# Performance work log

Measured on AMD Instinct MI355X. Metric: run time of the kernel, lower is better.

The kernel has to match this reference:

```python
import jax, jax.numpy as jnp
import numpy as np

B, S, E, H = 32, 512, 256, 256


def _slstm_scan(x, m, Wx, Wh, Ws, b, Us, Uh, bs):
    """x: [S,B,E], m: [S,B]. Returns per-step (h, c, s) each [S,B,H]."""
    Bn = x.shape[1]
    Hn = Wh.shape[0]
    z0 = jnp.zeros((Bn, Hn), x.dtype)

    def step(carry, xm):
        h, c, s = carry
        xt, mt = xm
        mt = mt[:, None]
        z = xt @ Wx + h @ Wh + s @ Ws + b  # [B, 4H]
        i, f, g, o = jnp.split(z, 4, axis=-1)
        c_new = jax.nn.sigmoid(f) * c + jax.nn.sigmoid(i) * jnp.tanh(g)
        h_new = jax.nn.sigmoid(o) * jnp.tanh(c_new)
        s_new = jnp.tanh(s @ Us + h_new @ Uh + bs)  # sentence-state message update
        h = mt * h_new + (1.0 - mt) * h
        c = mt * c_new + (1.0 - mt) * c
        s = mt * s_new + (1.0 - mt) * s
        return (h, c, s), (h, c, s)

    _, ys = jax.lax.scan(step, (z0, z0, z0), (x, m))
    return ys


def setup_inputs() -> dict:
    key = jax.random.key(0)
    ks = jax.random.split(key, 16)
    sc = 0.02
    d = {
        "inputs": jax.random.normal(ks[0], (B, S, E), jnp.float32),
        "mask": jnp.ones((B, S), jnp.float32),
        "idx": 1,
    }
    names = ["Wx", "Wh", "Ws", "b", "Us", "Uh", "bs"]
    shapes = [(E, 4 * H), (H, 4 * H), (H, 4 * H), (4 * H,), (H, H), (H, H), (H,)]
    k = 1
    for suf in ["_f", "_r"]:
        for n, sh in zip(names, shapes):
            d[n + suf] = sc * jax.random.normal(ks[k], sh, jnp.float32)
            k += 1
    return d


def reference(inputs, mask, idx,
              Wx_f, Wh_f, Ws_f, b_f, Us_f, Uh_f, bs_f,
              Wx_r, Wh_r, Ws_r, b_r, Us_r, Uh_r, bs_r):
    x = jnp.transpose(inputs, (1, 0, 2))  # [S,B,E]
    m = jnp.transpose(mask, (1, 0))       # [S,B]
    # forward direction
    h_f, c_f, s_f = _slstm_scan(x, m, Wx_f, Wh_f, Ws_f, b_f, Us_f, Uh_f, bs_f)
    # backward direction: scan over reversed time, then flip back to original order
    h_r, c_r, s_r = _slstm_scan(x[::-1], m[::-1], Wx_r, Wh_r, Ws_r, b_r, Us_r, Uh_r, bs_r)
    h_r, c_r, s_r = h_r[::-1], c_r[::-1], s_r[::-1]
    h_out = jnp.concatenate([h_f, h_r], axis=2)  # [S,B,2H]
    c_out = jnp.concatenate([c_f, c_r], axis=2)
    s_out = jnp.concatenate([s_f, s_r], axis=2)  # share=1 -> single stacked sentence-state tensor
    return (h_out, c_out, s_out)
```

## Files before the change

### kernel.cpp

```cpp
#include <hip/hip_runtime.h>
#include <stdint.h>

#define BB   32
#define SS   512
#define EE   256
#define HH   256
#define H4   1024
#define NTHR 512

#define NSD  8
#define SW   32

typedef short bf16x8 __attribute__((ext_vector_type(8)));
typedef float f32x4  __attribute__((ext_vector_type(4)));
typedef unsigned short u16x4 __attribute__((ext_vector_type(4)));
typedef unsigned long long ull;

#define F_HF  0
#define F_SF  16384
#define F_ZB  32768
#define F_US  49664
#define F_UH  53888
#define F_MB  58112
#define F_SMEM 58384

#define O_HF  0
#define O_SF  16384
#define O_XB  32768
#define O_ZB  49152
#define O_US  57344
#define O_UH  59392
#define O_CB  61440
#define O_MB  63488
#define O_SMEM 63744

__device__ __forceinline__ float bf2f(uint32_t u) {
  union { uint32_t i; float f; } v; v.i = u << 16; return v.f;
}
__device__ __forceinline__ uint32_t f2bf(float f) {
  union { float f; uint32_t i; } v; v.f = f;
  return (v.i + 0x7fffu + ((v.i >> 16) & 1u)) >> 16;
}
__device__ __forceinline__ float sigm(float x) { return 1.f / (1.f + __expf(-x)); }
__device__ __forceinline__ float tanhfast(float x) {
  float e = __expf(2.f * x);
  return 1.f - 2.f / (1.f + e);
}
__device__ __forceinline__ int fragAddr(int m, int k) {
  return (((m >> 4) * 8 + (k >> 5)) << 10) + (((m & 15) + (((k >> 3) & 3) << 4)) << 4) + ((k & 7) << 1);
}
__device__ __forceinline__ f32x4 mfma16(bf16x8 a, bf16x8 b, f32x4 c) {
  return __builtin_amdgcn_mfma_f32_16x16x32_bf16(a, b, c, 0, 0, 0);
}
__device__ __forceinline__ uint32_t blend2(uint32_t nw, uint32_t ow, float mv) {
  float b0 = mv * bf2f(nw & 0xffffu) + (1.f - mv) * bf2f(ow & 0xffffu);
  float b1 = mv * bf2f(nw >> 16)     + (1.f - mv) * bf2f(ow >> 16);
  return (f2bf(b0) & 0xffffu) | (f2bf(b1) << 16);
}

__device__ __forceinline__ void consume_tagged(const ull* __restrict__ src,
                                               char* dstBase, int sl, int lane, uint32_t tg,
                                               bool blendNow, const float* mbv,
                                               bool doStash, uint32_t* stash) {
  const int Lg = lane >> 3;
  const int c0 = (lane & 7) * 2;
  ull dA[4], dB[4];
  bool ok = false;
  while (!ok) {
    ok = true;
    #pragma unroll
    for (int i = 0; i < 4; ++i) {
      const int W = i * 128 + lane * 2;
      dA[i] = __hip_atomic_load(&src[W],     __ATOMIC_RELAXED, __HIP_MEMORY_SCOPE_AGENT);
      dB[i] = __hip_atomic_load(&src[W + 1], __ATOMIC_RELAXED, __HIP_MEMORY_SCOPE_AGENT);
    }
    #pragma unroll
    for (int i = 0; i < 4; ++i) {
      ok &= (((uint32_t)(dA[i] >> 16) & 0xffffu) == tg) & ((uint32_t)(dA[i] >> 48) == tg);
      ok &= (((uint32_t)(dB[i] >> 16) & 0xffffu) == tg) & ((uint32_t)(dB[i] >> 48) == tg);
    }
  }
  #pragma unroll
  for (int i = 0; i < 4; ++i) {
    const int m = i * 8 + Lg;
    uint32_t wa = ((uint32_t)dA[i] & 0xffffu) | (((uint32_t)dB[i] & 0xffffu) << 16);
    uint32_t wb = ((uint32_t)(dA[i] >> 32) & 0xffffu) | (((uint32_t)(dB[i] >> 32) & 0xffffu) << 16);
    char* pa = dstBase + (((m >> 4) * 8 + sl) << 10) + (((m & 15) + 16 * (c0 >> 3)) << 4) + (c0 & 7) * 2;
    char* pb = pa + 512;
    if (doStash) { stash[i * 2] = *(const uint32_t*)pa; stash[i * 2 + 1] = *(const uint32_t*)pb; }
    if (blendNow) {
      const float mv = mbv[m];
      wa = blend2(wa, *(const uint32_t*)pa, mv);
      wb = blend2(wb, *(const uint32_t*)pb, mv);
    }
    *(uint32_t*)pa = wa;
    *(uint32_t*)pb = wb;
  }
}

__device__ __forceinline__ void reblend_tagged(char* dstBase, int sl, int lane,
                                               const float* mbv, const uint32_t* stash) {
  const int Lg = lane >> 3;
  const int c0 = (lane & 7) * 2;
  #pragma unroll
  for (int i = 0; i < 4; ++i) {
    const int m = i * 8 + Lg;
    char* pa = dstBase + (((m >> 4) * 8 + sl) << 10) + (((m & 15) + 16 * (c0 >> 3)) << 4) + (c0 & 7) * 2;
    char* pb = pa + 512;
    const float mv = mbv[m];
    *(uint32_t*)pa = blend2(*(const uint32_t*)pa, stash[i * 2],     mv);
    *(uint32_t*)pb = blend2(*(const uint32_t*)pb, stash[i * 2 + 1], mv);
  }
}

__global__ void init_flags(uint32_t* f) {
  int i = blockIdx.x * blockDim.x + threadIdx.x;
  if (i < 1024) f[i] = 0u;
}
__global__ void zero_words(uint32_t* p, int n) {
  int i = blockIdx.x * blockDim.x + threadIdx.x;
  if (i < n) p[i] = 0u;
}

__global__ void __launch_bounds__(512)
xz_prepass(const float* __restrict__ x,
           const float* __restrict__ Wx_f, const float* __restrict__ b_f,
           const float* __restrict__ Wx_r, const float* __restrict__ b_r,
           unsigned short* __restrict__ xz) {
  __shared__ __align__(16) char smem[65536];
  const int bid = blockIdx.x;
  const int dir = bid >> 7;
  const int t0  = (bid & 127) * 4;
  const int tid = threadIdx.x;
  const int w = tid >> 6, lane = tid & 63;
  const int lr = lane & 15, lq = lane >> 4;
  const float* W  = dir ? Wx_r : Wx_f;
  const float* bv = dir ? b_r  : b_f;

  {
    const int bm = tid >> 4, e0 = (tid & 15) * 16;
    for (int tt = 0; tt < 4; ++tt) {
      const float* xs = x + ((size_t)bm * SS + (t0 + tt)) * EE + e0;
      float xr[16];
      #pragma unroll
      for (int i = 0; i < 16; ++i) xr[i] = xs[i];
      #pragma unroll
      for (int hfi = 0; hfi < 2; ++hfi) {
        bf16x8 vv;
        #pragma unroll
        for (int i = 0; i < 8; ++i) vv[i] = (short)f2bf(xr[hfi * 8 + i]);
        *(bf16x8*)(smem + tt * 16384 + fragAddr(bm, e0 + hfi * 8)) = vv;
      }
    }
  }
  __syncthreads();

  for (int j = 0; j < 8; ++j) {
    const int col = (w * 8 + j) * 16 + lr;
    const float breg = bv[col];
    f32x4 acc[4][2];
    #pragma unroll
    for (int tt = 0; tt < 4; ++tt)
      #pragma unroll
      for (int m = 0; m < 2; ++m) {
        acc[tt][m][0] = breg; acc[tt][m][1] = breg;
        acc[tt][m][2] = breg; acc[tt][m][3] = breg;
      }
    #pragma unroll
    for (int kk = 0; kk < 8; ++kk) {
      bf16x8 bfr;
      #pragma unroll
      for (int i = 0; i < 8; ++i)
        bfr[i] = (short)f2bf(W[(size_t)(kk * 32 + lq * 8 + i) * H4 + col]);
      #pragma unroll
      for (int tt = 0; tt < 4; ++tt) {
        bf16x8 a0 = *(const bf16x8*)(smem + tt * 16384 + (kk << 10) + lane * 16);
        bf16x8 a1 = *(const bf16x8*)(smem + tt * 16384 + ((8 + kk) << 10) + lane * 16);
        acc[tt][0] = mfma16(a0, bfr, acc[tt][0]);
        acc[tt][1] = mfma16(a1, bfr, acc[tt][1]);
      }
    }
    #pragma unroll
    for (int tt = 0; tt < 4; ++tt)
      #pragma unroll
      for (int m = 0; m < 2; ++m) {
        u16x4 pk;
        #pragma unroll
        for (int i = 0; i < 4; ++i) pk[i] = (unsigned short)f2bf(acc[tt][m][i]);
        *(u16x4*)(xz + (((size_t)dir * SS + (t0 + tt)) * H4 + col) * BB + m * 16 + lq * 4) = pk;
      }
  }
}

__global__ void __launch_bounds__(NTHR)
slstm_fast4(const float* __restrict__ mask,
            const float* Wh_f, const float* Ws_f,
            const float* Us_f, const float* Uh_f, const float* bs_f,
            const float* Wh_r, const float* Ws_r,
            const float* Us_r, const float* Uh_r, const float* bs_r,
            const unsigned short* __restrict__ xz,
            float* __restrict__ out,
            ull* __restrict__ hT, ull* __restrict__ sT) {
  __shared__ __align__(16) char smem[F_SMEM];

  const int bid = blockIdx.x;
  const int dir = bid >> 3;
  const int sid = bid & 7;
  const int tid = threadIdx.x;
  const int w = tid >> 6;
  const int lane = tid & 63;
  const int lr = lane & 15, lq = lane >> 4;
  const int mt = w & 1, q = w >> 1;

  const float* Wh = dir ? Wh_r : Wh_f;
  const float* Ws = dir ? Ws_r : Ws_f;
  const float* Us = dir ? Us_r : Us_f;
  const float* Uh = dir ? Uh_r : Uh_f;
  const float* bs = dir ? bs_r : bs_f;

  bf16x8 WhF[2][8], WsF[2][8], UF[8];
  #pragma unroll
  for (int nt = 0; nt < 2; ++nt) {
    const int col = q * HH + sid * SW + nt * 16 + lr;
    #pragma unroll
    for (int kk = 0; kk < 8; ++kk) {
      bf16x8 vh, vs;
      #pragma unroll
      for (int i = 0; i < 8; ++i) {
        const int k = kk * 32 + lq * 8 + i;
        vh[i] = (short)f2bf(Wh[(size_t)k * H4 + col]);
        vs[i] = (short)f2bf(Ws[(size_t)k * H4 + col]);
      }
      WhF[nt][kk] = vh; WsF[nt][kk] = vs;
    }
  }
  const int mtU = (w & 3) >> 1, ntU = w & 1;
  {
    const float* U = (w < 4) ? Us : Uh;
    const int colU = sid * SW + ntU * 16 + lr;
    #pragma unroll
    for (int kk = 0; kk < 8; ++kk) {
      bf16x8 vu;
      #pragma unroll
      for (int i = 0; i < 8; ++i) {
        const int k = kk * 32 + lq * 8 + i;
        vu[i] = (short)f2bf(U[(size_t)k * HH + colU]);
      }
      UF[kk] = vu;
    }
  }
  const float bs0 = bs[sid * SW + (tid & 15)];
  const float bs1 = bs[sid * SW + (tid & 15) + 16];

  {
    uint4* p = (uint4*)smem;
    for (int i = tid; i < 2048; i += NTHR) p[i] = make_uint4(0u, 0u, 0u, 0u);
  }
  const int ta0 = dir ? (SS - 1) : 0;
  {
    float mr = 0.f;
    if (tid < 32) mr = mask[(size_t)tid * SS + ta0];
    if (w == 0) {
      if (tid < 32) ((float*)(smem + F_MB))[tid] = mr;
      bool p = (lane < 32) ? (mr == 1.f) : true;
      ull bal = __ballot(p);
      if (lane == 0) ((int*)(smem + F_MB + 256))[0] = (bal == ~0ull) ? 1 : 0;
    }
  }
  const int zc0 = q * HH + sid * SW + lr;
  f32x4 accZ0, accZ1;
  {
    u16x4 xa = *(const u16x4*)(xz + (((size_t)dir * SS + ta0) * H4 + zc0) * BB + mt * 16 + lq * 4);
    u16x4 xb = *(const u16x4*)(xz + (((size_t)dir * SS + ta0) * H4 + zc0 + 16) * BB + mt * 16 + lq * 4);
    #pragma unroll
    for (int i = 0; i < 4; ++i) { accZ0[i] = bf2f(xa[i]); accZ1[i] = bf2f(xb[i]); }
  }
  float c0reg = 0.f, c1reg = 0.f;
  __syncthreads();

  const int m = tid >> 4, cc = tid & 15;
  const int mtL = m >> 4, rr = m & 15;

  for (int t = 0; t < SS; ++t) {
    const int par = t & 1;
    const float* mb  = (const float*)(smem + F_MB) + par * 32;
    const float* mbp = (const float*)(smem + F_MB) + (par ^ 1) * 32;
    const bool ao  = ((const int*)(smem + F_MB + 256))[par] != 0;
    const bool aop = ((const int*)(smem + F_MB + 256))[par ^ 1] != 0;

    if (t > 0 && w != sid) {
      const ull* src = sT + (size_t)(dir * NSD + w) * 512;
      consume_tagged(src, smem + F_SF, w, lane, (uint32_t)t, !aop, mbp, false, nullptr);
    }
    __syncthreads();

    #pragma unroll
    for (int kk = 0; kk < 8; ++kk) {
      bf16x8 as = *(const bf16x8*)(smem + F_SF + ((mt * 8 + kk) << 10) + lane * 16);
      accZ0 = mfma16(as, WsF[0][kk], accZ0);
      accZ1 = mfma16(as, WsF[1][kk], accZ1);
    }
    {
      float* zb = (float*)(smem + F_ZB);
      const int base = (mt * 4 + q) * 528;
      #pragma unroll
      for (int i = 0; i < 4; ++i) {
        zb[base + (lq * 4 + i) * 33 + lr]      = accZ0[i];
        zb[base + (lq * 4 + i) * 33 + 16 + lr] = accZ1[i];
      }
    }
    __syncthreads();

    float hbl0, hbl1;
    {
      const float* zb = (const float*)(smem + F_ZB);
      float hn0, hn1;
      #pragma unroll
      for (int half = 0; half < 2; ++half) {
        const int n = cc + half * 16;
        const float zi = zb[(0 * 2 + mtL) * 2 * 528 / 2 + 0];
        (void)zi;
        const float z_i = zb[(mtL * 4 + 0) * 528 + rr * 33 + n];
        const float z_f = zb[(mtL * 4 + 1) * 528 + rr * 33 + n];
        const float z_g = zb[(mtL * 4 + 2) * 528 + rr * 33 + n];
        const float z_o = zb[(mtL * 4 + 3) * 528 + rr * 33 + n];
        const float cold = half ? c1reg : c0reg;
        const float cn = sigm(z_f) * cold + sigm(z_i) * tanhfast(z_g);
        const float hn = sigm(z_o) * tanhfast(cn);
        float cblv, hblv;
        if (ao) { cblv = cn; hblv = hn; }
        else {
          const float mval = mb[m];
          cblv = mval * cn + (1.f - mval) * cold;
          const float hold = bf2f(*(const uint16_t*)(smem + F_HF + fragAddr(m, sid * SW + n)));
          hblv = mval * hn + (1.f - mval) * hold;
        }
        if (half == 0) { c0reg = cblv; hn0 = hn; hbl0 = hblv; }
        else           { c1reg = cblv; hn1 = hn; hbl1 = hblv; }
      }
      const uint32_t tg = (uint32_t)(t + 1);
      ull pub = (ull)((f2bf(hn0) & 0xffffu) | (tg << 16))
              | ((ull)((f2bf(hn1) & 0xffffu) | (tg << 16)) << 32);
      __hip_atomic_store(&hT[(size_t)(dir * NSD + sid) * 512 + m * 16 + cc], pub,
                         __ATOMIC_RELAXED, __HIP_MEMORY_SCOPE_AGENT);
      if (ao) {
        uint32_t hb0 = f2bf(hn0), hb1 = f2bf(hn1);
        uint32_t p0 = (uint32_t)__shfl_xor((int)hb0, 1);
        uint32_t p1 = (uint32_t)__shfl_xor((int)hb1, 1);
        if (!(cc & 1)) {
          *(uint32_t*)(smem + F_HF + fragAddr(m, sid * SW + cc))      = (hb0 & 0xffffu) | (p0 << 16);
          *(uint32_t*)(smem + F_HF + fragAddr(m, sid * SW + cc + 16)) = (hb1 & 0xffffu) | (p1 << 16);
        }
      }
    }

    const int tact = dir ? (SS - 1 - t) : t;
    {
      const size_t ob = ((size_t)tact * BB + m) * (2 * HH) + (size_t)dir * HH + sid * SW + cc;
      __builtin_nontemporal_store(hbl0, &out[ob]);
      __builtin_nontemporal_store(hbl1, &out[ob + 16]);
      const float cb0 = c0reg, cb1 = c1reg;
      __builtin_nontemporal_store(cb0, &out[ob + 8388608]);
      __builtin_nontemporal_store(cb1, &out[ob + 16 + 8388608]);
    }
    u16x4 nxa = {0, 0, 0, 0}, nxb = {0, 0, 0, 0};
    if (t + 1 < SS) {
      const int ta = dir ? (SS - 2 - t) : (t + 1);
      nxa = *(const u16x4*)(xz + (((size_t)dir * SS + ta) * H4 + zc0) * BB + mt * 16 + lq * 4);
      nxb = *(const u16x4*)(xz + (((size_t)dir * SS + ta) * H4 + zc0 + 16) * BB + mt * 16 + lq * 4);
      float mr = 0.f;
      if (tid < 32) mr = mask[(size_t)tid * SS + ta];
      if (w == 0) {
        if (tid < 32) ((float*)(smem + F_MB))[(par ^ 1) * 32 + tid] = mr;
        bool p = (lane < 32) ? (mr == 1.f) : true;
        ull bal = __ballot(p);
        if (lane == 0) ((int*)(smem + F_MB + 256))[par ^ 1] = (bal == ~0ull) ? 1 : 0;
      }
    }
    if (w < 4) {
      f32x4 accU = {0.f, 0.f, 0.f, 0.f};
      #pragma unroll
      for (int kk = 0; kk < 8; ++kk) {
        bf16x8 as = *(const bf16x8*)(smem + F_SF + ((mtU * 8 + kk) << 10) + lane * 16);
        accU = mfma16(as, UF[kk], accU);
      }
      float* us = (float*)(smem + F_US);
      #pragma unroll
      for (int i = 0; i < 4; ++i)
        us[(mtU * 16 + lq * 4 + i) * 33 + ntU * 16 + lr] = accU[i];
    }

    if (!ao) __syncthreads();
    uint32_t stOld[8];
    if (!(ao && w == sid)) {
      const ull* src = hT + (size_t)(dir * NSD + w) * 512;
      consume_tagged(src, smem + F_HF, w, lane, (uint32_t)(t + 1), false, nullptr, !ao, stOld);
    }
    __syncthreads();

    if (w >= 4) {
      f32x4 accU = {0.f, 0.f, 0.f, 0.f};
      #pragma unroll
      for (int kk = 0; kk < 8; ++kk) {
        bf16x8 ah = *(const bf16x8*)(smem + F_HF + ((mtU * 8 + kk) << 10) + lane * 16);
        accU = mfma16(ah, UF[kk], accU);
      }
      float* uh = (float*)(smem + F_UH);
      #pragma unroll
      for (int i = 0; i < 4; ++i)
        uh[(mtU * 16 + lq * 4 + i) * 33 + ntU * 16 + lr] = accU[i];
    }
    __syncthreads();
    if (!ao) {
      reblend_tagged(smem + F_HF, w, lane, mb, stOld);
      __syncthreads();
    }

    {
      const float* us = (const float*)(smem + F_US);
      const float* uh = (const float*)(smem + F_UH);
      const float sv0 = us[m * 33 + cc]      + uh[m * 33 + cc]      + bs0;
      const float sv1 = us[m * 33 + cc + 16] + uh[m * 33 + cc + 16] + bs1;
      const float sn0 = tanhfast(sv0);
      const float sn1 = tanhfast(sv1);
      if (t + 1 < SS) {
        const uint32_t tg = (uint32_t)(t + 1);
        ull pub = (ull)((f2bf(sn0) & 0xffffu) | (tg << 16))
                | ((ull)((f2bf(sn1) & 0xffffu) | (tg << 16)) << 32);
        __hip_atomic_store(&sT[(size_t)(dir * NSD + sid) * 512 + m * 16 + cc], pub,
                           __ATOMIC_RELAXED, __HIP_MEMORY_SCOPE_AGENT);
      }
      float sbl0 = sn0, sbl1 = sn1;
      if (!ao) {
        const float mval = mb[m];
        const float so0 = bf2f(*(const uint16_t*)(smem + F_SF + fragAddr(m, sid * SW + cc)));
        const float so1 = bf2f(*(const uint16_t*)(smem + F_SF + fragAddr(m, sid * SW + cc + 16)));
        sbl0 = mval * sn0 + (1.f - mval) * so0;
        sbl1 = mval * sn1 + (1.f - mval) * so1;
      }
      const size_t obS = ((size_t)tact * BB + m) * (2 * HH) + (size_t)dir * HH + sid * SW + cc + 16777216;
      __builtin_nontemporal_store(sbl0, &out[obS]);
      __builtin_nontemporal_store(sbl1, &out[obS + 16]);
      uint32_t sb0 = f2bf(sbl0), sb1 = f2bf(sbl1);
      uint32_t p0 = (uint32_t)__shfl_xor((int)sb0, 1);
      uint32_t p1 = (uint32_t)__shfl_xor((int)sb1, 1);
      if (!(cc & 1)) {
        *(uint32_t*)(smem + F_SF + fragAddr(m, sid * SW + cc))      = (sb0 & 0xffffu) | (p0 << 16);
        *(uint32_t*)(smem + F_SF + fragAddr(m, sid * SW + cc + 16)) = (sb1 & 0xffffu) | (p1 << 16);
      }
    }

    if (t + 1 < SS) {
      f32x4 aZ0, aZ1;
      #pragma unroll
      for (int i = 0; i < 4; ++i) { aZ0[i] = bf2f(nxa[i]); aZ1[i] = bf2f(nxb[i]); }
      #pragma unroll
      for (int kk = 0; kk < 8; ++kk) {
        bf16x8 ah = *(const bf16x8*)(smem + F_HF + ((mt * 8 + kk) << 10) + lane * 16);
        aZ0 = mfma16(ah, WhF[0][kk], aZ0);
        aZ1 = mfma16(ah, WhF[1][kk], aZ1);
      }
      accZ0 = aZ0; accZ1 = aZ1;
    }
  }
}

__global__ void __launch_bounds__(NTHR)
slstm_persistent(const float* __restrict__ x, const float* __restrict__ mask,
                 const float* Wx_f, const float* Wh_f, const float* Ws_f, const float* b_f,
                 const float* Us_f, const float* Uh_f, const float* bs_f,
                 const float* Wx_r, const float* Wh_r, const float* Ws_r, const float* b_r,
                 const float* Us_r, const float* Uh_r, const float* bs_r,
                 float* __restrict__ out, uint32_t* __restrict__ wsbase) {
  __shared__ __align__(16) char smem[O_SMEM];

  const int bid = blockIdx.x;
  const int dir = bid >> 4;
  const int g   = bid & 15;
  const int tid = threadIdx.x;
  const int w    = tid >> 6;
  const int lane = tid & 63;
  const int lr = lane & 15, lq = lane >> 4;
  const int mt = w & 1;
  const int q  = w >> 1;

  const float* Wx = dir ? Wx_r : Wx_f;
  const float* Wh = dir ? Wh_r : Wh_f;
  const float* Ws = dir ? Ws_r : Ws_f;
  const float* bv = dir ? b_r  : b_f;
  const float* Us = dir ? Us_r : Us_f;
  const float* Uh = dir ? Uh_r : Uh_f;
  const float* bs = dir ? bs_r : bs_f;

  uint32_t* flags = wsbase;
  uint32_t* hbufB = wsbase + 1024;
  uint32_t* sbufB = wsbase + 1024 + 16384;
  uint32_t* flagH = flags + (dir * 2 + 0) * 16 * 16;
  uint32_t* flagS = flags + (dir * 2 + 1) * 16 * 16;

  bf16x8 WxF[8], WhF[8], WsF[8], UF[8];
  {
    const int col = q * HH + g * 16 + lr;
    #pragma unroll
    for (int kk = 0; kk < 8; ++kk) {
      bf16x8 vx, vh, vs;
      #pragma unroll
      for (int i = 0; i < 8; ++i) {
        int k = kk * 32 + lq * 8 + i;
        vx[i] = (short)f2bf(Wx[k * H4 + col]);
        vh[i] = (short)f2bf(Wh[k * H4 + col]);
        vs[i] = (short)f2bf(Ws[k * H4 + col]);
      }
      WxF[kk] = vx; WhF[kk] = vh; WsF[kk] = vs;
    }
  }
  if (w < 4) {
    const float* U = (w < 2) ? Us : Uh;
    const int colU = g * 16 + lr;
    #pragma unroll
    for (int kk = 0; kk < 8; ++kk) {
      bf16x8 vu;
      #pragma unroll
      for (int i = 0; i < 8; ++i) {
        int k = kk * 32 + lq * 8 + i;
        vu[i] = (short)f2bf(U[k * HH + colU]);
      }
      UF[kk] = vu;
    }
  }
  const float breg  = bv[q * HH + g * 16 + lr];
  const float bsreg = bs[g * 16 + (tid & 15)];

  {
    uint4* p = (uint4*)(smem);
    for (int i = tid; i < 2048; i += NTHR) p[i] = make_uint4(0u, 0u, 0u, 0u);
    float* cb = (float*)(smem + O_CB);
    for (int i = tid; i < BB * 16; i += NTHR) cb[i] = 0.f;
  }
  {
    const int ta = dir ? (SS - 1) : 0;
    const int bm = tid >> 4, e0 = (tid & 15) * 16;
    const float* xs = x + ((size_t)bm * SS + ta) * EE + e0;
    float xr0[16];
    #pragma unroll
    for (int i = 0; i < 16; ++i) xr0[i] = xs[i];
    #pragma unroll
    for (int hfi = 0; hfi < 2; ++hfi) {
      bf16x8 vv;
      #pragma unroll
      for (int i = 0; i < 8; ++i) vv[i] = (short)f2bf(xr0[hfi * 8 + i]);
      *(bf16x8*)(smem + O_XB + fragAddr(bm, e0 + hfi * 8)) = vv;
    }
    if (tid < BB) ((float*)(smem + O_MB))[tid] = mask[(size_t)tid * SS + ta];
  }
  __syncthreads();

  for (int t = 0; t < SS; ++t) {
    const int par = t & 1;
    uint32_t* HbufP = hbufB + (dir * 2 + par) * (16 * 256);
    uint32_t* SbufP = sbufB + (dir * 2 + par) * (16 * 256);
    const float* mb = (const float*)(smem + O_MB + par * 128);

    f32x4 accZ; accZ[0] = breg; accZ[1] = breg; accZ[2] = breg; accZ[3] = breg;
    f32x4 accU = {0.f, 0.f, 0.f, 0.f};
    #pragma unroll
    for (int kk = 0; kk < 8; ++kk) {
      const int fb = ((mt * 8 + kk) << 10) + lane * 16;
      bf16x8 ah = *(const bf16x8*)(smem + O_HF + fb);
      bf16x8 as = *(const bf16x8*)(smem + O_SF + fb);
      bf16x8 ax = *(const bf16x8*)(smem + O_XB + fb);
      accZ = mfma16(ax, WxF[kk], accZ);
      accZ = mfma16(ah, WhF[kk], accZ);
      accZ = mfma16(as, WsF[kk], accZ);
      if (w < 2) accU = mfma16(as, UF[kk], accU);
    }

    float xr[16]; float mreg = 0.f;
    if (t + 1 < SS) {
      const int ta = dir ? (SS - 2 - t) : (t + 1);
      const int bm = tid >> 4, e0 = (tid & 15) * 16;
      const float* xs = x + ((size_t)bm * SS + ta) * EE + e0;
      #pragma unroll
      for (int i = 0; i < 16; ++i) xr[i] = xs[i];
      if (tid < BB) mreg = mask[(size_t)tid * SS + ta];
    }

    {
      float* zb = (float*)(smem + O_ZB);
      #pragma unroll
      for (int i = 0; i < 4; ++i)
        zb[(mt * 4 + q) * 256 + (lq * 4 + i) * 16 + lr] = accZ[i];
      if (w < 2) {
        float* ub = (float*)(smem + O_US);
        #pragma unroll
        for (int i = 0; i < 4; ++i)
          ub[mt * 256 + (lq * 4 + i) * 16 + lr] = accU[i];
      }
    }
    __syncthreads();

    const int bm = tid >> 4, cc = tid & 15;
    const int mtL = bm >> 4, rr = bm & 15;
    float mval;
    {
      const float* zb = (const float*)(smem + O_ZB);
      float zi = zb[(mtL * 4 + 0) * 256 + rr * 16 + cc];
      float zf = zb[(mtL * 4 + 1) * 256 + rr * 16 + cc];
      float zg = zb[(mtL * 4 + 2) * 256 + rr * 16 + cc];
      float zo = zb[(mtL * 4 + 3) * 256 + rr * 16 + cc];
      float* cb = (float*)(smem + O_CB);
      float cold = cb[bm * 16 + cc];
      mval = mb[bm];
      float cn = sigm(zf) * cold + sigm(zi) * tanhfast(zg);
      float hnew = sigm(zo) * tanhfast(cn);
      float cbl = mval * cn + (1.f - mval) * cold;
      cb[bm * 16 + cc] = cbl;
      float hold = bf2f(*(const uint16_t*)(smem + O_HF + fragAddr(bm, g * 16 + cc)));
      float hbl = mval * hnew + (1.f - mval) * hold;
      const int tact = dir ? (SS - 1 - t) : t;
      size_t ob = ((size_t)tact * BB + bm) * (2 * HH) + (size_t)dir * HH + g * 16 + cc;
      out[ob] = hbl;
      out[ob + 8388608] = cbl;
      uint32_t hb = f2bf(hnew);
      uint32_t pv = (uint32_t)__shfl_xor((int)hb, 1);
      if ((tid & 1) == 0) {
        uint32_t word = (hb & 0xffffu) | (pv << 16);
        __hip_atomic_store(&HbufP[g * 256 + (tid >> 1)], word,
                           __ATOMIC_RELAXED, __HIP_MEMORY_SCOPE_AGENT);
      }
    }
    __syncthreads();
    if (tid == 0)
      __hip_atomic_store(&flagH[g * 16], (uint32_t)(t + 1),
                         __ATOMIC_RELAXED, __HIP_MEMORY_SCOPE_AGENT);

    uint32_t oldw[2][4];
    #pragma unroll
    for (int ssl = 0; ssl < 2; ++ssl) {
      const int sl = w + ssl * 8;
      if (lane == 0) {
        while (__hip_atomic_load(&flagH[sl * 16], __ATOMIC_RELAXED,
                                 __HIP_MEMORY_SCOPE_AGENT) < (uint32_t)(t + 1)) {}
      }
      const uint32_t* src = HbufP + sl * 256;
      #pragma unroll
      for (int ww = 0; ww < 4; ++ww) {
        const int word = ww * 64 + lane;
        uint32_t v = __hip_atomic_load(&src[word], __ATOMIC_RELAXED, __HIP_MEMORY_SCOPE_AGENT);
        const int mrow = word >> 3, c0 = (word & 7) * 2;
        const int fa = fragAddr(mrow, sl * 16 + c0);
        oldw[ssl][ww] = *(uint32_t*)(smem + O_HF + fa);
        *(uint32_t*)(smem + O_HF + fa) = v;
      }
    }
    __syncthreads();

    if (w == 2 || w == 3) {
      f32x4 aU = {0.f, 0.f, 0.f, 0.f};
      #pragma unroll
      for (int kk = 0; kk < 8; ++kk) {
        bf16x8 ah = *(const bf16x8*)(smem + O_HF + (((w & 1) * 8 + kk) << 10) + lane * 16);
        aU = mfma16(ah, UF[kk], aU);
      }
      float* ub = (float*)(smem + O_UH);
      #pragma unroll
      for (int i = 0; i < 4; ++i)
        ub[(w & 1) * 256 + (lq * 4 + i) * 16 + lr] = aU[i];
    }
    __syncthreads();

    #pragma unroll
    for (int ssl = 0; ssl < 2; ++ssl) {
      const int sl = w + ssl * 8;
      #pragma unroll
      for (int ww = 0; ww < 4; ++ww) {
        const int word = ww * 64 + lane;
        const int mrow = word >> 3, c0 = (word & 7) * 2;
        const int fa = fragAddr(mrow, sl * 16 + c0);
        uint32_t nv = *(uint32_t*)(smem + O_HF + fa);
        uint32_t ov = oldw[ssl][ww];
        float mv = mb[mrow];
        *(uint32_t*)(smem + O_HF + fa) = blend2(nv, ov, mv);
      }
    }
    {
      const float* ub1 = (const float*)(smem + O_US);
      const float* ub2 = (const float*)(smem + O_UH);
      float sv = ub1[mtL * 256 + rr * 16 + cc] + ub2[mtL * 256 + rr * 16 + cc] + bsreg;
      float snew = tanhfast(sv);
      float sold = bf2f(*(const uint16_t*)(smem + O_SF + fragAddr(bm, g * 16 + cc)));
      float sbl = mval * snew + (1.f - mval) * sold;
      const int tact = dir ? (SS - 1 - t) : t;
      out[((size_t)tact * BB + bm) * (2 * HH) + (size_t)dir * HH + g * 16 + cc + 16777216] = sbl;
      uint32_t sb = f2bf(snew);
      uint32_t pv = (uint32_t)__shfl_xor((int)sb, 1);
      if ((tid & 1) == 0) {
        uint32_t word = (sb & 0xffffu) | (pv << 16);
        __hip_atomic_store(&SbufP[g * 256 + (tid >> 1)], word,
                           __ATOMIC_RELAXED, __HIP_MEMORY_SCOPE_AGENT);
      }
    }
    __syncthreads();
    if (tid == 0)
      __hip_atomic_store(&flagS[g * 16], (uint32_t)(t + 1),
                         __ATOMIC_RELAXED, __HIP_MEMORY_SCOPE_AGENT);

    #pragma unroll
    for (int ssl = 0; ssl < 2; ++ssl) {
      const int sl = w + ssl * 8;
      if (lane == 0) {
        while (__hip_atomic_load(&flagS[sl * 16], __ATOMIC_RELAXED,
                                 __HIP_MEMORY_SCOPE_AGENT) < (uint32_t)(t + 1)) {}
      }
      const uint32_t* src = SbufP + sl * 256;
      #pragma unroll
      for (int ww = 0; ww < 4; ++ww) {
        const int word = ww * 64 + lane;
        uint32_t v = __hip_atomic_load(&src[word], __ATOMIC_RELAXED, __HIP_MEMORY_SCOPE_AGENT);
        const int mrow = word >> 3, c0 = (word & 7) * 2;
        const int fa = fragAddr(mrow, sl * 16 + c0);
        uint32_t ov = *(uint32_t*)(smem + O_SF + fa);
        float mv = mb[mrow];
        *(uint32_t*)(smem + O_SF + fa) = blend2(v, ov, mv);
      }
    }
    if (t + 1 < SS) {
      const int bm2 = tid >> 4, e0 = (tid & 15) * 16;
      #pragma unroll
      for (int hfi = 0; hfi < 2; ++hfi) {
        bf16x8 vv;
        #pragma unroll
        for (int i = 0; i < 8; ++i) vv[i] = (short)f2bf(xr[hfi * 8 + i]);
        *(bf16x8*)(smem + O_XB + fragAddr(bm2, e0 + hfi * 8)) = vv;
      }
      float* mbn = (float*)(smem + O_MB + ((t + 1) & 1) * 128);
      if (tid < BB) mbn[tid] = mreg;
    }
    __syncthreads();
  }
}

extern "C" void kernel_launch(void* const* d_in, const int* in_sizes, int n_in,
                              void* d_out, int out_size, void* d_ws, size_t ws_size,
                              hipStream_t stream) {
  (void)in_sizes; (void)n_in; (void)out_size;
  const float* x    = (const float*)d_in[0];
  const float* mask = (const float*)d_in[1];
  const float* Wx_f = (const float*)d_in[3];
  const float* Wh_f = (const float*)d_in[4];
  const float* Ws_f = (const float*)d_in[5];
  const float* b_f  = (const float*)d_in[6];
  const float* Us_f = (const float*)d_in[7];
  const float* Uh_f = (const float*)d_in[8];
  const float* bs_f = (const float*)d_in[9];
  const float* Wx_r = (const float*)d_in[10];
  const float* Wh_r = (const float*)d_in[11];
  const float* Ws_r = (const float*)d_in[12];
  const float* b_r  = (const float*)d_in[13];
  const float* Us_r = (const float*)d_in[14];
  const float* Uh_r = (const float*)d_in[15];
  const float* bs_r = (const float*)d_in[16];
  float* out = (float*)d_out;
  uint32_t* ws = (uint32_t*)d_ws;

  const size_t XZ_WORDS = (size_t)2 * SS * H4 * BB / 2;
  const size_t TBUF_ULL = (size_t)2 * NSD * 512;
  const size_t need = XZ_WORDS * 4 + 2 * TBUF_ULL * 8;

  if (ws_size >= need) {
    unsigned short* xz = (unsigned short*)ws;
    ull* hT = (ull*)(ws + XZ_WORDS);
    ull* sT = hT + TBUF_ULL;
    zero_words<<<dim3(128), dim3(256), 0, stream>>>((uint32_t*)hT, (int)(2 * TBUF_ULL * 2));
    xz_prepass<<<dim3(256), dim3(512), 0, stream>>>(x, Wx_f, b_f, Wx_r, b_r, xz);
    slstm_fast4<<<dim3(16), dim3(NTHR), 0, stream>>>(
        mask, Wh_f, Ws_f, Us_f, Uh_f, bs_f,
        Wh_r, Ws_r, Us_r, Uh_r, bs_r, xz, out, hT, sT);
  } else {
    init_flags<<<dim3(4), dim3(256), 0, stream>>>(ws);
    slstm_persistent<<<dim3(32), dim3(NTHR), 0, stream>>>(
        x, mask, Wx_f, Wh_f, Ws_f, b_f, Us_f, Uh_f, bs_f,
        Wx_r, Wh_r, Ws_r, b_r, Us_r, Uh_r, bs_r, out, ws);
  }
}
```

Measured before the change: 2.576 ms.

## Restructure input-projection prepass to keep Wx tiles in registers across timesteps

The prepass now assigns each block a column group and a 32-step time range, so each wave converts its Wx slice to bf16 once, keeps it in registers, and loops over timesteps, prefetching the next x row with float4 loads. The old layout re-read and re-converted Wx from global memory for every 4-timestep block. The reverse direction processes time in descending order, likely so its xz rows become ready in the order the recurrent kernel consumes them. Sigmoid and tanh now use the hardware reciprocal instead of a full divide, and a dead LDS load is removed, trading some accuracy for fewer instructions on the recurrence's critical path.

```diff
diff --git a/kernel.cpp b/kernel.cpp
--- a/kernel.cpp
+++ b/kernel.cpp
@@ -41,10 +41,11 @@
   union { float f; uint32_t i; } v; v.f = f;
   return (v.i + 0x7fffu + ((v.i >> 16) & 1u)) >> 16;
 }
-__device__ __forceinline__ float sigm(float x) { return 1.f / (1.f + __expf(-x)); }
+__device__ __forceinline__ float sigm(float x) {
+  return __builtin_amdgcn_rcpf(1.f + __expf(-x));
+}
 __device__ __forceinline__ float tanhfast(float x) {
-  float e = __expf(2.f * x);
-  return 1.f - 2.f / (1.f + e);
+  return 1.f - 2.f * __builtin_amdgcn_rcpf(1.f + __expf(2.f * x));
 }
 __device__ __forceinline__ int fragAddr(int m, int k) {
   return (((m >> 4) * 8 + (k >> 5)) << 10) + (((m & 15) + (((k >> 3) & 3) << 4)) << 4) + ((k & 7) << 1);
@@ -123,72 +124,95 @@
 }
 
 __global__ void __launch_bounds__(512)
-xz_prepass(const float* __restrict__ x,
-           const float* __restrict__ Wx_f, const float* __restrict__ b_f,
-           const float* __restrict__ Wx_r, const float* __restrict__ b_r,
-           unsigned short* __restrict__ xz) {
-  __shared__ __align__(16) char smem[65536];
+xz_prepass2(const float* __restrict__ x,
+            const float* __restrict__ Wx_f, const float* __restrict__ b_f,
+            const float* __restrict__ Wx_r, const float* __restrict__ b_r,
+            unsigned short* __restrict__ xz) {
+  __shared__ __align__(16) char smem[16384];
   const int bid = blockIdx.x;
   const int dir = bid >> 7;
-  const int t0  = (bid & 127) * 4;
+  const int cg  = (bid >> 4) & 7;
+  const int tg  = bid & 15;
   const int tid = threadIdx.x;
   const int w = tid >> 6, lane = tid & 63;
   const int lr = lane & 15, lq = lane >> 4;
   const float* W  = dir ? Wx_r : Wx_f;
   const float* bv = dir ? b_r  : b_f;
 
+  const int col = (cg * 8 + w) * 16 + lr;
+  const float breg = bv[col];
+
+  bf16x8 WxT[8];
+  #pragma unroll
+  for (int kk = 0; kk < 8; ++kk) {
+    bf16x8 v;
+    #pragma unroll
+    for (int i = 0; i < 8; ++i)
+      v[i] = (short)f2bf(W[(size_t)(kk * 32 + lq * 8 + i) * H4 + col]);
+    WxT[kk] = v;
+  }
+
+  const int bm = tid >> 4, e0 = (tid & 15) * 16;
   {
-    const int bm = tid >> 4, e0 = (tid & 15) * 16;
-    for (int tt = 0; tt < 4; ++tt) {
-      const float* xs = x + ((size_t)bm * SS + (t0 + tt)) * EE + e0;
-      float xr[16];
-      #pragma unroll
-      for (int i = 0; i < 16; ++i) xr[i] = xs[i];
-      #pragma unroll
-      for (int hfi = 0; hfi < 2; ++hfi) {
-        bf16x8 vv;
-        #pragma unroll
-        for (int i = 0; i < 8; ++i) vv[i] = (short)f2bf(xr[hfi * 8 + i]);
-        *(bf16x8*)(smem + tt * 16384 + fragAddr(bm, e0 + hfi * 8)) = vv;
-      }
-    }
+    const int ta = dir ? (511 - tg * 32) : (tg * 32);
+    const float4* xs4 = (const float4*)(x + ((size_t)bm * SS + ta) * EE + e0);
+    float xr[16];
+    #pragma unroll
+    for (int v4 = 0; v4 < 4; ++v4) {
+      float4 xv = xs4[v4];
+      xr[v4 * 4 + 0] = xv.x; xr[v4 * 4 + 1] = xv.y;
+      xr[v4 * 4 + 2] = xv.z; xr[v4 * 4 + 3] = xv.w;
+    }
+    bf16x8 v0, v1;
+    #pragma unroll
+    for (int i = 0; i < 8; ++i) { v0[i] = (short)f2bf(xr[i]); v1[i] = (short)f2bf(xr[8 + i]); }
+    *(bf16x8*)(smem + fragAddr(bm, e0))     = v0;
+    *(bf16x8*)(smem + fragAddr(bm, e0 + 8)) = v1;
   }
   __syncthreads();
 
-  for (int j = 0; j < 8; ++j) {
-    const int col = (w * 8 + j) * 16 + lr;
-    const float breg = bv[col];
-    f32x4 acc[4][2];
-    #pragma unroll
-    for (int tt = 0; tt < 4; ++tt)
-      #pragma unroll
-      for (int m = 0; m < 2; ++m) {
-        acc[tt][m][0] = breg; acc[tt][m][1] = breg;
-        acc[tt][m][2] = breg; acc[tt][m][3] = breg;
-      }
+  for (int ti = 0; ti < 32; ++ti) {
+    const int ta = dir ? (511 - tg * 32 - ti) : (tg * 32 + ti);
+    float xr[16];
+    if (ti + 1 < 32) {
+      const int tn = dir ? (ta - 1) : (ta + 1);
+      const float4* xs4 = (const float4*)(x + ((size_t)bm * SS + tn) * EE + e0);
+      #pragma unroll
+      for (int v4 = 0; v4 < 4; ++v4) {
+        float4 xv = xs4[v4];
+        xr[v4 * 4 + 0] = xv.x; xr[v4 * 4 + 1] = xv.y;
+        xr[v4 * 4 + 2] = xv.z; xr[v4 * 4 + 3] = xv.w;
+      }
+    }
+    f32x4 acc0 = {breg, breg, breg, breg};
+    f32x4 acc1 = {breg, breg, breg, breg};
     #pragma unroll
     for (int kk = 0; kk < 8; ++kk) {
-      bf16x8 bfr;
-      #pragma unroll
-      for (int i = 0; i < 8; ++i)
-        bfr[i] = (short)f2bf(W[(size_t)(kk * 32 + lq * 8 + i) * H4 + col]);
-      #pragma unroll
-      for (int tt = 0; tt < 4; ++tt) {
-        bf16x8 a0 = *(const bf16x8*)(smem + tt * 16384 + (kk << 10) + lane * 16);
-        bf16x8 a1 = *(const bf16x8*)(smem + tt * 16384 + ((8 + kk) << 10) + lane * 16);
-        acc[tt][0] = mfma16(a0, bfr, acc[tt][0]);
-        acc[tt][1] = mfma16(a1, bfr, acc[tt][1]);
-      }
-    }
-    #pragma unroll
-    for (int tt = 0; tt < 4; ++tt)
-      #pragma unroll
-      for (int m = 0; m < 2; ++m) {
-        u16x4 pk;
-        #pragma unroll
-        for (int i = 0; i < 4; ++i) pk[i] = (unsigned short)f2bf(acc[tt][m][i]);
-        *(u16x4*)(xz + (((size_t)dir * SS + (t0 + tt)) * H4 + col) * BB + m * 16 + lq * 4) = pk;
-      }
+      bf16x8 a0 = *(const bf16x8*)(smem + (kk << 10) + lane * 16);
+      bf16x8 a1 = *(const bf16x8*)(smem + ((8 + kk) << 10) + lane * 16);
+      acc0 = mfma16(a0, WxT[kk], acc0);
+      acc1 = mfma16(a1, WxT[kk], acc1);
+    }
+    {
+      u16x4 p0, p1;
+      #pragma unroll
+      for (int i = 0; i < 4; ++i) {
+        p0[i] = (unsigned short)f2bf(acc0[i]);
+        p1[i] = (unsigned short)f2bf(acc1[i]);
+      }
+      unsigned short* dst = xz + ((size_t)(dir * SS + ta) * H4 + col) * BB + lq * 4;
+      *(u16x4*)dst        = p0;
+      *(u16x4*)(dst + 16) = p1;
+    }
+    __syncthreads();
+    if (ti + 1 < 32) {
+      bf16x8 v0, v1;
+      #pragma unroll
+      for (int i = 0; i < 8; ++i) { v0[i] = (short)f2bf(xr[i]); v1[i] = (short)f2bf(xr[8 + i]); }
+      *(bf16x8*)(smem + fragAddr(bm, e0))     = v0;
+      *(bf16x8*)(smem + fragAddr(bm, e0 + 8)) = v1;
+    }
+    __syncthreads();
   }
 }
 
@@ -318,8 +342,6 @@
       #pragma unroll
       for (int half = 0; half < 2; ++half) {
         const int n = cc + half * 16;
-        const float zi = zb[(0 * 2 + mtL) * 2 * 528 / 2 + 0];
-        (void)zi;
         const float z_i = zb[(mtL * 4 + 0) * 528 + rr * 33 + n];
         const float z_f = zb[(mtL * 4 + 1) * 528 + rr * 33 + n];
         const float z_g = zb[(mtL * 4 + 2) * 528 + rr * 33 + n];
@@ -772,7 +794,7 @@
     ull* hT = (ull*)(ws + XZ_WORDS);
     ull* sT = hT + TBUF_ULL;
     zero_words<<<dim3(128), dim3(256), 0, stream>>>((uint32_t*)hT, (int)(2 * TBUF_ULL * 2));
-    xz_prepass<<<dim3(256), dim3(512), 0, stream>>>(x, Wx_f, b_f, Wx_r, b_r, xz);
+    xz_prepass2<<<dim3(256), dim3(512), 0, stream>>>(x, Wx_f, b_f, Wx_r, b_r, xz);
     slstm_fast4<<<dim3(16), dim3(NTHR), 0, stream>>>(
         mask, Wh_f, Ws_f, Us_f, Uh_f, bs_f,
         Wh_r, Ws_r, Us_r, Uh_r, bs_r, xz, out, hT, sT);
```

Result: faster. 2.237 ms (-13.2%).
